# Kernel optimization log

Hardware: AMD Instinct MI355X
Metric: run time of the kernel (lower is better)

The kernel has to match this reference:

```python
import jax, jax.numpy as jnp
import numpy as np

EMBED_DIM = 64   # conv out channels / linear in features
PATCH_DIM = 64   # linear out features
KSIZE, STRIDE, PAD = 5, 2, 2
B, T = 4, 480000


def setup_inputs() -> dict:
    key = jax.random.key(0)
    k1, k2, k3, k4, k5 = jax.random.split(key, 5)
    audio_waveform = jax.random.normal(k1, (B, T), jnp.float32)
    # conv1d weights: [out_ch, in_ch, k]
    conv_w = jax.random.normal(k2, (EMBED_DIM, 1, KSIZE), jnp.float32) / np.sqrt(KSIZE).astype(np.float32)
    conv_b = 0.01 * jax.random.normal(k3, (EMBED_DIM,), jnp.float32)
    # linear patch encoder: [patch_dim, embed_dim] (torch convention W @ x)
    lin_w = jax.random.normal(k4, (PATCH_DIM, EMBED_DIM), jnp.float32) / np.sqrt(EMBED_DIM).astype(np.float32)
    lin_b = 0.01 * jax.random.normal(k5, (PATCH_DIM,), jnp.float32)
    return dict(audio_waveform=audio_waveform, conv_w=conv_w, conv_b=conv_b,
                lin_w=lin_w, lin_b=lin_b)


def reference(audio_waveform, conv_w, conv_b, lin_w, lin_b):
    # [B, T] -> [B, 1, T]
    x = audio_waveform[:, None, :]
    # Conv1d(1 -> EMBED_DIM, k=5, stride=2, pad=2): [B, E, T//2]
    feats = jax.lax.conv_general_dilated(
        x, conv_w, window_strides=(STRIDE,), padding=[(PAD, PAD)],
        dimension_numbers=('NCH', 'OIH', 'NCH'))
    feats = jax.nn.relu(feats + conv_b[None, :, None])
    feats = feats.transpose(0, 2, 1)  # [B, seq_len, E]
    # Per-timestep linear patch encoder. NOTE: the torch module's
    # entropy-gated segmentation loop only chooses patch boundaries;
    # since patches are re-concatenated in order and the Linear is
    # applied per timestep, the output is exactly this, for any
    # entropy predictor / threshold.
    return jnp.einsum('bse,pe->bsp', feats, lin_w) + lin_b
```

## Files before the change

### kernel.cpp

```cpp
#include <hip/hip_runtime.h>
#include <hip/hip_bf16.h>
#include <stdint.h>

#define B_SZ    4
#define T_LEN   480000
#define S_LEN   240000
#define KS      5
#define TPB     15000
#define NTILES  (B_SZ * TPB)
#define GRID    512

typedef __attribute__((ext_vector_type(8))) __bf16  bf16x8;
typedef __attribute__((ext_vector_type(4))) float   f32x4;

__global__ __launch_bounds__(256) void audio_enc_kernel(
    const float* __restrict__ audio,
    const float* __restrict__ conv_w,
    const float* __restrict__ conv_b,
    const float* __restrict__ lin_w,
    const float* __restrict__ lin_b,
    float* __restrict__ out)
{
  const int lane = threadIdx.x & 63;
  const int m    = lane & 15;
  const int q    = lane >> 4;
  const int wid  = threadIdx.x >> 6;
  const int wv   = (int)((blockIdx.x << 2) | wid);
  const int nw   = (int)(gridDim.x << 2);

  __shared__ float lds[4][1024];
  float* const lw = lds[wid];

  float cw[2][8][KS], cbv[2][8];
#pragma unroll
  for (int h = 0; h < 2; ++h)
#pragma unroll
    for (int j = 0; j < 8; ++j) {
      const int e = h * 32 + q * 8 + j;
#pragma unroll
      for (int t = 0; t < KS; ++t) cw[h][j][t] = conv_w[e * KS + t];
      cbv[h][j] = conv_b[e];
    }

  bf16x8 wfrag[2][4];
#pragma unroll
  for (int nt = 0; nt < 4; ++nt) {
    const int p = nt * 16 + m;
#pragma unroll
    for (int kt = 0; kt < 2; ++kt) {
      const float* src = lin_w + p * 64 + kt * 32 + q * 8;
#pragma unroll
      for (int j = 0; j < 8; ++j) wfrag[kt][nt][j] = (__bf16)src[j];
    }
  }

  f32x4 lb4[4];
#pragma unroll
  for (int nt = 0; nt < 4; ++nt)
    lb4[nt] = *reinterpret_cast<const f32x4*>(lin_b + nt * 16 + q * 4);

  if (wv >= NTILES) return;
  int b  = wv / TPB;
  int sb = wv - b * TPB;

  auto load_tile = [&](int bb, int s0, float2& A, float2& Bv, float& C) {
    const float* base = audio + (size_t)bb * T_LEN;
    const int sl = s0 + m;
    const int gi = 2 * sl - 2;
    A = *reinterpret_cast<const float2*>(base + (gi < 0 ? 0 : gi));
    if (gi < 0) { A.x = 0.f; A.y = 0.f; }
    Bv = *reinterpret_cast<const float2*>(base + 2 * sl);
    const int ci = 2 * sl + 2;
    const float cv = base[ci < T_LEN ? ci : T_LEN - 1];
    C = (ci < T_LEN) ? cv : 0.f;
  };

  float2 fa, fb; float c1;
  load_tile(b, sb * 16, fa, fb, c1);

  while (true) {
    const float x0 = fa.x, x1 = fa.y, x2 = fb.x, x3 = fb.y, x4 = c1;
    const int bc = b, s0 = sb * 16;

    int sbn = sb + nw, bn = b;
    if (sbn >= TPB) { sbn -= TPB; ++bn; }
    const bool more = (bn < B_SZ);
    if (more) load_tile(bn, sbn * 16, fa, fb, c1);

    bf16x8 xf[2];
#pragma unroll
    for (int h = 0; h < 2; ++h)
#pragma unroll
      for (int j = 0; j < 8; ++j) {
        float a = cbv[h][j];
        a = fmaf(cw[h][j][0], x0, a);
        a = fmaf(cw[h][j][1], x1, a);
        a = fmaf(cw[h][j][2], x2, a);
        a = fmaf(cw[h][j][3], x3, a);
        a = fmaf(cw[h][j][4], x4, a);
        a = fmaxf(a, 0.f);
        xf[h][j] = (__bf16)a;
      }

#pragma unroll
    for (int nt = 0; nt < 4; ++nt) {
      f32x4 acc = lb4[nt];
      acc = __builtin_amdgcn_mfma_f32_16x16x32_bf16(wfrag[0][nt], xf[0], acc, 0, 0, 0);
      acc = __builtin_amdgcn_mfma_f32_16x16x32_bf16(wfrag[1][nt], xf[1], acc, 0, 0, 0);
      *reinterpret_cast<f32x4*>(lw + m * 64 + ((nt * 16 + q * 4) ^ (m << 2))) = acc;
    }

    float* ob = out + ((size_t)bc * S_LEN + (size_t)s0) * 64;
#pragma unroll
    for (int g = 0; g < 4; ++g) {
      const int r = g * 4 + q;
      const f32x4 v = *reinterpret_cast<const f32x4*>(
          lw + r * 64 + ((m << 2) ^ (r << 2)));
      *reinterpret_cast<f32x4*>(ob + g * 256 + lane * 4) = v;
    }

    if (!more) break;
    b = bn; sb = sbn;
  }
}

extern "C" void kernel_launch(void* const* d_in, const int* in_sizes, int n_in,
                              void* d_out, int out_size, void* d_ws, size_t ws_size,
                              hipStream_t stream) {
  const float* audio  = (const float*)d_in[0];
  const float* conv_w = (const float*)d_in[1];
  const float* conv_b = (const float*)d_in[2];
  const float* lin_w  = (const float*)d_in[3];
  const float* lin_b  = (const float*)d_in[4];
  float* out = (float*)d_out;

  audio_enc_kernel<<<dim3(GRID), dim3(256), 0, stream>>>(
      audio, conv_w, conv_b, lin_w, lin_b, out);
}
```

Baseline: 262.2 us.

## Move conv weights to LDS, add bias at store, double grid for occupancy

Conv weights now sit in shared memory and are read as vector loads each iteration instead of being held in 80 registers per thread. The linear bias is added during the LDS-to-global copy, so the per-tile bias fragments are no longer kept in registers. The grid doubles to 1024 blocks and launch bounds now ask for 4 blocks per CU, aiming for more waves in flight on this store-bound kernel. The trade-off is extra LDS reads per tile and a barrier at startup.

```diff
diff --git a/kernel.cpp b/kernel.cpp
--- a/kernel.cpp
+++ b/kernel.cpp
@@ -8,12 +8,14 @@
 #define KS      5
 #define TPB     15000
 #define NTILES  (B_SZ * TPB)
-#define GRID    512
+#define GRID    1024
+
+static_assert(4 * GRID <= TPB, "single-wrap batch advance requires nw <= TPB");
 
 typedef __attribute__((ext_vector_type(8))) __bf16  bf16x8;
 typedef __attribute__((ext_vector_type(4))) float   f32x4;
 
-__global__ __launch_bounds__(256) void audio_enc_kernel(
+__global__ __launch_bounds__(256, 4) void audio_enc_kernel(
     const float* __restrict__ audio,
     const float* __restrict__ conv_w,
     const float* __restrict__ conv_b,
@@ -28,19 +30,20 @@
   const int wv   = (int)((blockIdx.x << 2) | wid);
   const int nw   = (int)(gridDim.x << 2);
 
-  __shared__ float lds[4][1024];
-  float* const lw = lds[wid];
+  __shared__ __align__(16) float w_lds[KS][64];
+  __shared__ __align__(16) float stage[4][1024];
+  float* const lw = stage[wid];
 
-  float cw[2][8][KS], cbv[2][8];
+  for (int idx = threadIdx.x; idx < 64 * KS; idx += 256) {
+    const int e = idx / KS, t = idx - e * KS;
+    w_lds[t][e] = conv_w[idx];
+  }
+
+  float cbv[2][8];
 #pragma unroll
   for (int h = 0; h < 2; ++h)
 #pragma unroll
-    for (int j = 0; j < 8; ++j) {
-      const int e = h * 32 + q * 8 + j;
-#pragma unroll
-      for (int t = 0; t < KS; ++t) cw[h][j][t] = conv_w[e * KS + t];
-      cbv[h][j] = conv_b[e];
-    }
+    for (int j = 0; j < 8; ++j) cbv[h][j] = conv_b[h * 32 + q * 8 + j];
 
   bf16x8 wfrag[2][4];
 #pragma unroll
@@ -54,10 +57,9 @@
     }
   }
 
-  f32x4 lb4[4];
-#pragma unroll
-  for (int nt = 0; nt < 4; ++nt)
-    lb4[nt] = *reinterpret_cast<const f32x4*>(lin_b + nt * 16 + q * 4);
+  const f32x4 bias4 = *reinterpret_cast<const f32x4*>(lin_b + m * 4);
+
+  __syncthreads();
 
   if (wv >= NTILES) return;
   int b  = wv / TPB;
@@ -87,24 +89,34 @@
     const bool more = (bn < B_SZ);
     if (more) load_tile(bn, sbn * 16, fa, fb, c1);
 
+    float a0[8], a1[8];
+#pragma unroll
+    for (int j = 0; j < 8; ++j) { a0[j] = cbv[0][j]; a1[j] = cbv[1][j]; }
+    const float xs[KS] = {x0, x1, x2, x3, x4};
+#pragma unroll
+    for (int t5 = 0; t5 < KS; ++t5) {
+      const f32x4 wa0 = *reinterpret_cast<const f32x4*>(&w_lds[t5][q * 8]);
+      const f32x4 wb0 = *reinterpret_cast<const f32x4*>(&w_lds[t5][q * 8 + 4]);
+      const f32x4 wa1 = *reinterpret_cast<const f32x4*>(&w_lds[t5][32 + q * 8]);
+      const f32x4 wb1 = *reinterpret_cast<const f32x4*>(&w_lds[t5][32 + q * 8 + 4]);
+#pragma unroll
+      for (int j = 0; j < 4; ++j) {
+        a0[j]     = fmaf(wa0[j], xs[t5], a0[j]);
+        a0[j + 4] = fmaf(wb0[j], xs[t5], a0[j + 4]);
+        a1[j]     = fmaf(wa1[j], xs[t5], a1[j]);
+        a1[j + 4] = fmaf(wb1[j], xs[t5], a1[j + 4]);
+      }
+    }
     bf16x8 xf[2];
 #pragma unroll
-    for (int h = 0; h < 2; ++h)
-#pragma unroll
-      for (int j = 0; j < 8; ++j) {
-        float a = cbv[h][j];
-        a = fmaf(cw[h][j][0], x0, a);
-        a = fmaf(cw[h][j][1], x1, a);
-        a = fmaf(cw[h][j][2], x2, a);
-        a = fmaf(cw[h][j][3], x3, a);
-        a = fmaf(cw[h][j][4], x4, a);
-        a = fmaxf(a, 0.f);
-        xf[h][j] = (__bf16)a;
-      }
+    for (int j = 0; j < 8; ++j) {
+      xf[0][j] = (__bf16)fmaxf(a0[j], 0.f);
+      xf[1][j] = (__bf16)fmaxf(a1[j], 0.f);
+    }
 
 #pragma unroll
     for (int nt = 0; nt < 4; ++nt) {
-      f32x4 acc = lb4[nt];
+      f32x4 acc = {0.f, 0.f, 0.f, 0.f};
       acc = __builtin_amdgcn_mfma_f32_16x16x32_bf16(wfrag[0][nt], xf[0], acc, 0, 0, 0);
       acc = __builtin_amdgcn_mfma_f32_16x16x32_bf16(wfrag[1][nt], xf[1], acc, 0, 0, 0);
       *reinterpret_cast<f32x4*>(lw + m * 64 + ((nt * 16 + q * 4) ^ (m << 2))) = acc;
@@ -114,8 +126,9 @@
 #pragma unroll
     for (int g = 0; g < 4; ++g) {
       const int r = g * 4 + q;
-      const f32x4 v = *reinterpret_cast<const f32x4*>(
+      f32x4 v = *reinterpret_cast<const f32x4*>(
           lw + r * 64 + ((m << 2) ^ (r << 2)));
+      v = v + bias4;
       *reinterpret_cast<f32x4*>(ob + g * 256 + lane * 4) = v;
     }
 
```

After: 370.3 us. +41.2%, slower.
